# Performance work log

Measured on AMD Instinct MI355X. Metric: run time of the kernel, lower is better.

Reference implementation:

```python
import jax, jax.numpy as jnp
import numpy as np

B, N, T, F_FEAT, T_OUT = 256, 512, 12, 12, 12
HID = 3 * N           # 1536, LSTM hidden size
IN = N * F_FEAT       # 6144, LSTM input size


def setup_inputs() -> dict:
    key = jax.random.key(0)
    ks = jax.random.split(key, 8)
    stdv = 1.0 / np.sqrt(HID)
    u = lambda k, shape, s: jax.random.uniform(k, shape, jnp.float32, -s, s)
    return {
        "A_hat": jax.random.normal(ks[0], (N, N), jnp.float32),
        "X": jax.random.normal(ks[1], (B, N, T, F_FEAT), jnp.float32),
        "W_ih": u(ks[2], (4 * HID, IN), stdv),
        "W_hh": u(ks[3], (4 * HID, HID), stdv),
        "b_ih": u(ks[4], (4 * HID,), stdv),
        "b_hh": u(ks[5], (4 * HID,), stdv),
        "lin_W": u(ks[6], (T_OUT, 3 * T), 1.0 / np.sqrt(3 * T)),
        "lin_b": u(ks[7], (T_OUT,), 1.0 / np.sqrt(3 * T)),
    }


def reference(A_hat, X, W_ih, W_hh, b_ih, b_hh, lin_W, lin_b):
    # (B, N, T, F) -> (B, N*T, F) -> (F, B, N*T); loop axis is the feature dim
    out1 = X.reshape(B, N * T, F_FEAT).transpose(2, 0, 1)

    def step(carry, x_t):  # x_t: (B, N*T)
        h, c = carry
        gates = x_t @ W_ih.T + b_ih + h @ W_hh.T + b_hh  # (B, 4*HID)
        i, f, g, o = jnp.split(gates, 4, axis=-1)        # PyTorch gate order i,f,g,o
        c = jax.nn.sigmoid(f) * c + jax.nn.sigmoid(i) * jnp.tanh(g)
        h = jax.nn.sigmoid(o) * jnp.tanh(c)
        h = jnp.tanh(h)  # extra tanh applied in the original forward
        return (h, c), h

    init = (jnp.zeros((B, HID), X.dtype), jnp.zeros((B, HID), X.dtype))
    _, hs = jax.lax.scan(step, init, out1)          # (F, B, HID)
    al = hs.transpose(1, 2, 0)                      # (B, 3N, F) == torch.cat of unsqueezed states
    out2 = al.reshape(B, N, 3 * T)                  # (B, N, 3T)
    out3 = jax.nn.relu(out2) @ lin_W.T + lin_b      # (B, N, T_OUT)
    return out3
```

## Files before the change

kernel.cpp:

```cpp
#include <hip/hip_runtime.h>
#include <hip/hip_bf16.h>
#include <stdint.h>

typedef uint16_t u16;
typedef __attribute__((ext_vector_type(8))) __bf16 bf16x8;
typedef __attribute__((ext_vector_type(4))) float f32x4;
typedef __attribute__((ext_vector_type(4))) u16 u16x4;

#define BSZ   256
#define NN    512
#define TT    12
#define FF    12
#define HID   1536
#define INSZ  6144
#define GATES 6144
#define MROWS 3072

static __device__ __forceinline__ u16 f2bf(float x) {
  uint32_t u = __builtin_bit_cast(uint32_t, x);
  u += 0x7fffu + ((u >> 16) & 1u);
  return (u16)(u >> 16);
}

static __device__ __forceinline__ float sigm(float x) {
  return 1.0f / (1.0f + expf(-x));
}

__global__ void cvt_perm(const float* __restrict__ in, u16* __restrict__ out,
                         int ncol4) {
  long idx = (long)blockIdx.x * blockDim.x + threadIdx.x;
  int r  = (int)(idx / ncol4);
  int c4 = (int)(idx - (long)r * ncol4);
  int rp = ((r % HID) << 2) + r / HID;
  float4 v = ((const float4*)in)[idx];
  u16x4 w = { f2bf(v.x), f2bf(v.y), f2bf(v.z), f2bf(v.w) };
  ((u16x4*)out)[(size_t)rp * ncol4 + c4] = w;
}

__global__ void pack_x4(const float* __restrict__ X, u16* __restrict__ Ax) {
  int idx = blockIdx.x * blockDim.x + threadIdx.x;
  int b  = idx / (INSZ / 4);
  int k4 = idx - b * (INSZ / 4);
  const float* xp = X + (size_t)b * (INSZ * FF) + (size_t)k4 * (4 * FF);
  float4 v[12];
#pragma unroll
  for (int j = 0; j < 12; ++j) v[j] = ((const float4*)xp)[j];
  const float* vf = (const float*)v;
#pragma unroll
  for (int f = 0; f < FF; ++f) {
    u16x4 w = { f2bf(vf[0 * FF + f]), f2bf(vf[1 * FF + f]),
                f2bf(vf[2 * FF + f]), f2bf(vf[3 * FF + f]) };
    *(u16x4*)&Ax[(size_t)(f * BSZ + b) * INSZ + k4 * 4] = w;
  }
}

#define BM8 192
#define BN8 384
#define LDSA_SZ 24576
#define LDSB_SZ 49152
#define LDS_TOTAL (2 * (LDSA_SZ + LDSB_SZ))

#define GLL(src, dst)                                                          \
  __builtin_amdgcn_global_load_lds(                                            \
      (const __attribute__((address_space(1))) void*)(src),                    \
      (__attribute__((address_space(3))) void*)(dst), 16, 0, 0)

#define SBAR() asm volatile("s_barrier" ::: "memory")
#define SCHED_FENCE_DS() __builtin_amdgcn_sched_barrier(0x7F)
#define WAIT_LGKM0()                                                           \
  do {                                                                         \
    asm volatile("s_waitcnt lgkmcnt(0)" ::: "memory");                         \
    __builtin_amdgcn_sched_barrier(0);                                         \
  } while (0)

#define MFMA9(AF, BF, RO, CO)                                                  \
  do {                                                                         \
    __builtin_amdgcn_s_setprio(1);                                             \
    _Pragma("unroll") for (int i = 0; i < 3; ++i)                              \
        _Pragma("unroll") for (int j = 0; j < 3; ++j)                          \
            acc[RO + i][CO + j] = __builtin_amdgcn_mfma_f32_16x16x32_bf16(     \
                AF[i], BF[j], acc[RO + i][CO + j], 0, 0, 0);                   \
    __builtin_amdgcn_s_setprio(0);                                             \
  } while (0)

__global__ __launch_bounds__(512, 1) void gemm8p(
    const u16* __restrict__ A, const u16* __restrict__ Bt,
    const float* __restrict__ bi, const float* __restrict__ bh,
    float* __restrict__ C, int M, int N, int K) {
  extern __shared__ __align__(16) char lds[];
  const int tid  = threadIdx.x;
  const int lane = tid & 63;
  const int wid  = tid >> 6;
  const int wr   = wid >> 2;
  const int wc   = wid & 3;

  const int nbx  = N / BN8;
  const int cpx  = gridDim.x >> 3;
  const int orig = blockIdx.x;
  const int wgid = (orig & 7) * cpx + (orig >> 3);
  const int m0   = (wgid / nbx) * BM8;
  const int n0   = (wgid % nbx) * BN8;

  const int fr    = lane & 15;
  const int kb    = (lane >> 4) << 4;
  const int swz   = (fr & 7) << 4;
  const int colp0 = kb ^ swz;
  const int colp1 = (64 | kb) ^ swz;

  const int srow = tid >> 3;
  const int scb  = ((tid & 7) << 4) ^ ((srow & 7) << 4);
  const u16* gA = A  + (size_t)(m0 + srow) * K + (scb >> 1);
  const u16* gB = Bt + (size_t)(n0 + srow) * K + (scb >> 1);
  const int wdst = wid << 10;

  char* ldsA = lds;
  char* ldsB = lds + 2 * LDSA_SZ;
  char* aRowB = ldsA + (wr * 96 + fr) * 128;
  char* bRowB = ldsB + (wc * 96 + fr) * 128;

  f32x4 acc[6][6] = {};
  const int NT = K >> 6;

#pragma unroll
  for (int c = 0; c < 3; ++c) GLL(gA + (size_t)c * 64 * K, ldsA + c * 8192 + wdst);
#pragma unroll
  for (int c = 0; c < 6; ++c) GLL(gB + (size_t)c * 64 * K, ldsB + c * 8192 + wdst);

  for (int t = 0; t < NT; ++t) {
    const int p = t & 1;
    char* aRow = aRowB + p * LDSA_SZ;
    char* bRow = bRowB + p * LDSB_SZ;
    char* An = ldsA + (p ^ 1) * LDSA_SZ;
    char* Bn = ldsB + (p ^ 1) * LDSB_SZ;
    const u16* gAn = gA + (size_t)(t + 1) * 64;
    const u16* gBn = gB + (size_t)(t + 1) * 64;
    const bool pf = (t + 1 < NT);

    bf16x8 a0[2][3], a1[2][3], b0[2][3], b1[2][3];

    if (pf) {
#pragma unroll
      for (int c = 0; c < 3; ++c) GLL(gAn + (size_t)c * 64 * K, An + c * 8192 + wdst);
      asm volatile("s_waitcnt vmcnt(3)" ::: "memory");
    } else {
      asm volatile("s_waitcnt vmcnt(0)" ::: "memory");
    }
    SBAR();

#pragma unroll
    for (int i = 0; i < 3; ++i) {
      a0[0][i] = *(const bf16x8*)(aRow + i * 2048 + colp0);
      b0[0][i] = *(const bf16x8*)(bRow + i * 2048 + colp0);
    }
#pragma unroll
    for (int i = 0; i < 3; ++i) b1[0][i] = *(const bf16x8*)(bRow + (3 + i) * 2048 + colp0);
    MFMA9(a0[0], b0[0], 0, 0);
    if (pf) {
      GLL(gBn + (size_t)0 * 64 * K, Bn + 0 * 8192 + wdst);
      GLL(gBn + (size_t)1 * 64 * K, Bn + 1 * 8192 + wdst);
    }
    SCHED_FENCE_DS();

#pragma unroll
    for (int i = 0; i < 3; ++i) a1[0][i] = *(const bf16x8*)(aRow + (3 + i) * 2048 + colp0);
    MFMA9(a0[0], b1[0], 0, 3);
    if (pf) {
      GLL(gBn + (size_t)2 * 64 * K, Bn + 2 * 8192 + wdst);
      GLL(gBn + (size_t)3 * 64 * K, Bn + 3 * 8192 + wdst);
    }
    SCHED_FENCE_DS();

#pragma unroll
    for (int i = 0; i < 3; ++i) a0[1][i] = *(const bf16x8*)(aRow + i * 2048 + colp1);
    MFMA9(a1[0], b1[0], 3, 3);
    if (pf) {
      GLL(gBn + (size_t)4 * 64 * K, Bn + 4 * 8192 + wdst);
      GLL(gBn + (size_t)5 * 64 * K, Bn + 5 * 8192 + wdst);
    }
    SCHED_FENCE_DS();

#pragma unroll
    for (int i = 0; i < 3; ++i) b0[1][i] = *(const bf16x8*)(bRow + i * 2048 + colp1);
    MFMA9(a1[0], b0[0], 3, 0);
    SCHED_FENCE_DS();

#pragma unroll
    for (int i = 0; i < 3; ++i) b1[1][i] = *(const bf16x8*)(bRow + (3 + i) * 2048 + colp1);
    MFMA9(a0[1], b0[1], 0, 0);
    SCHED_FENCE_DS();

#pragma unroll
    for (int i = 0; i < 3; ++i) a1[1][i] = *(const bf16x8*)(aRow + (3 + i) * 2048 + colp1);
    MFMA9(a0[1], b1[1], 0, 3);
    SCHED_FENCE_DS();

    MFMA9(a1[1], b1[1], 3, 3);
    MFMA9(a1[1], b0[1], 3, 0);

    SBAR();
  }

  const int r0 = (lane >> 4) << 2;
  const int cc = lane & 15;
#pragma unroll
  for (int j = 0; j < 6; ++j) {
    const int col = n0 + wc * 96 + j * 16 + cc;
    const int oc  = (col & 3) * HID + (col >> 2);
    const float bv = bi[oc] + bh[oc];
#pragma unroll
    for (int i = 0; i < 6; ++i) {
      const size_t rbase = (size_t)(m0 + wr * 96 + i * 16 + r0) * N + col;
#pragma unroll
      for (int r = 0; r < 4; ++r)
        C[rbase + (size_t)r * N] = acc[i][j][r] + bv;
    }
  }
}

__global__ __launch_bounds__(256, 4) void gemm_cell(
    const u16* __restrict__ hbf_in,
    const u16* __restrict__ Whhb,
    const float* __restrict__ XW_f,
    float* __restrict__ cbuf,
    u16* __restrict__ hbf_out,
    float* __restrict__ hs_f) {
  __shared__ __align__(16) char lds[24576];
  const int tid  = threadIdx.x;
  const int lane = tid & 63;
  const int wid  = tid >> 6;
  const int wr   = wid >> 1;
  const int wc   = wid & 1;

  const int orig = blockIdx.x;
  const int xcd  = orig & 7;
  const int jj   = orig >> 3;
  const int n0   = (12 * xcd + (jj >> 3)) * 64;
  const int m0   = (jj & 7) * 32;
  const int K    = HID;

  const int fr    = lane & 15;
  const int kb    = (lane >> 4) << 4;
  const int swz   = (fr & 7) << 4;
  const int colp0 = kb ^ swz;
  const int colp1 = (64 | kb) ^ swz;

  const int srow = tid >> 3;
  const int scb  = ((tid & 7) << 4) ^ ((srow & 7) << 4);
  const u16* gA = hbf_in + (size_t)(m0 + srow) * K + (scb >> 1);
  const u16* gB = Whhb   + (size_t)(n0 + srow) * K + (scb >> 1);
  const int wdst = wid << 10;

  char* ldsA = lds;
  char* ldsB = lds + 8192;
  char* aRowB = ldsA + (wr * 16 + fr) * 128;
  char* bRowB = ldsB + (wc * 32 + fr) * 128;

  f32x4 acc[2] = {};
  const int NT = K >> 6;

  GLL(gA,                  ldsA + wdst);
  GLL(gB,                  ldsB + wdst);
  GLL(gB + (size_t)32 * K, ldsB + 4096 + wdst);

  for (int t = 0; t < NT; ++t) {
    const int p = t & 1;
    char* aRow = aRowB + p * 4096;
    char* bRow = bRowB + p * 8192;
    char* An = ldsA + (p ^ 1) * 4096;
    char* Bn = ldsB + (p ^ 1) * 8192;
    const u16* gAn = gA + (size_t)(t + 1) * 64;
    const u16* gBn = gB + (size_t)(t + 1) * 64;

    if (t + 1 < NT) {
      GLL(gAn,                  An + wdst);
      GLL(gBn,                  Bn + wdst);
      GLL(gBn + (size_t)32 * K, Bn + 4096 + wdst);
      asm volatile("s_waitcnt vmcnt(3)" ::: "memory");
    } else {
      asm volatile("s_waitcnt vmcnt(0)" ::: "memory");
    }
    SBAR();

    bf16x8 a[2], b[2][2];
    a[0] = *(const bf16x8*)(aRow + colp0);
    a[1] = *(const bf16x8*)(aRow + colp1);
#pragma unroll
    for (int j = 0; j < 2; ++j) {
      b[0][j] = *(const bf16x8*)(bRow + j * 2048 + colp0);
      b[1][j] = *(const bf16x8*)(bRow + j * 2048 + colp1);
    }
    WAIT_LGKM0();
    __builtin_amdgcn_s_setprio(1);
#pragma unroll
    for (int k = 0; k < 2; ++k)
#pragma unroll
      for (int j = 0; j < 2; ++j)
        acc[j] = __builtin_amdgcn_mfma_f32_16x16x32_bf16(a[k], b[k][j], acc[j], 0, 0, 0);
    __builtin_amdgcn_s_setprio(0);
    SBAR();
  }

  float* sacc = (float*)lds;
  const int r0 = (lane >> 4) << 2;
  const int cc = lane & 15;
#pragma unroll
  for (int j = 0; j < 2; ++j) {
    const int ml = wr * 16 + r0;
    const int nl = wc * 32 + j * 16 + cc;
#pragma unroll
    for (int r = 0; r < 4; ++r)
      sacc[(ml + r) * 68 + nl] = acc[j][r];
  }
  __syncthreads();

  for (int it = tid; it < 512; it += 256) {
    const int bl = it >> 4;
    const int jl = it & 15;
    const int b  = m0 + bl;
    const int jg = (n0 >> 2) + jl;
    const float4 hw = *(const float4*)&sacc[bl * 68 + jl * 4];
    const float4 xw = *(const float4*)&XW_f[(size_t)b * GATES + n0 + jl * 4];
    const float gi = xw.x + hw.x;
    const float gf = xw.y + hw.y;
    const float gg = xw.z + hw.z;
    const float go = xw.w + hw.w;
    const int cidx = b * HID + jg;
    const float cp = cbuf[cidx];
    const float cv = sigm(gf) * cp + sigm(gi) * tanhf(gg);
    const float h  = tanhf(sigm(go) * tanhf(cv));
    cbuf[cidx]    = cv;
    hbf_out[cidx] = f2bf(h);
    hs_f[cidx]    = h;
  }
}

__global__ void cell_first(const float* __restrict__ XW,
                           float* __restrict__ cbuf,
                           u16* __restrict__ hbf_out,
                           float* __restrict__ hs_f) {
  int it = blockIdx.x * blockDim.x + threadIdx.x;
  int b = it / HID;
  int j = it - b * HID;
  const float4 xw = *(const float4*)&XW[(size_t)b * GATES + 4 * j];
  const float cv = sigm(xw.x) * tanhf(xw.z);
  const float h  = tanhf(sigm(xw.w) * tanhf(cv));
  cbuf[it]    = cv;
  hbf_out[it] = f2bf(h);
  hs_f[it]    = h;
}

__global__ __launch_bounds__(256) void final_k(const float* __restrict__ hs,
                                               const float* __restrict__ lin_W,
                                               const float* __restrict__ lin_b,
                                               float* __restrict__ out) {
  __shared__ float Wsh[12 * 36];
  __shared__ float bsh[12];
  for (int i = threadIdx.x; i < 12 * 36; i += blockDim.x) Wsh[i] = lin_W[i];
  if (threadIdx.x < 12) bsh[threadIdx.x] = lin_b[threadIdx.x];
  __syncthreads();

  int idx = blockIdx.x * blockDim.x + threadIdx.x;
  int b = idx >> 9;
  int n = idx & 511;

  float acc[12];
#pragma unroll
  for (int o = 0; o < 12; ++o) acc[o] = bsh[o];

#pragma unroll
  for (int kk = 0; kk < 3; ++kk)
#pragma unroll
    for (int f = 0; f < 12; ++f) {
      float v = hs[(size_t)(f * BSZ + b) * HID + 3 * n + kk];
      v = fmaxf(v, 0.0f);
      int j = 12 * kk + f;
#pragma unroll
      for (int o = 0; o < 12; ++o) acc[o] += v * Wsh[o * 36 + j];
    }

#pragma unroll
  for (int o = 0; o < 12; ++o) out[(size_t)idx * 12 + o] = acc[o];
}

extern "C" void kernel_launch(void* const* d_in, const int* in_sizes, int n_in,
                              void* d_out, int out_size, void* d_ws, size_t ws_size,
                              hipStream_t stream) {
  (void)in_sizes; (void)n_in; (void)out_size; (void)ws_size;
  const float* X     = (const float*)d_in[1];
  const float* W_ih  = (const float*)d_in[2];
  const float* W_hh  = (const float*)d_in[3];
  const float* b_ih  = (const float*)d_in[4];
  const float* b_hh  = (const float*)d_in[5];
  const float* lin_W = (const float*)d_in[6];
  const float* lin_b = (const float*)d_in[7];
  float* out = (float*)d_out;

  char* p = (char*)d_ws;
  u16*   Ax   = (u16*)p;   p += (size_t)MROWS * INSZ * 2;
  u16*   Wihb = (u16*)p;   p += (size_t)GATES * INSZ * 2;
  u16*   Whhb = (u16*)p;   p += (size_t)GATES * HID * 2;
  float* XW   = (float*)p; p += (size_t)MROWS * GATES * 4;
  u16*   hbfA = (u16*)p;   p += (size_t)BSZ * HID * 2;
  u16*   hbfB = (u16*)p;   p += (size_t)BSZ * HID * 2;
  float* cbuf = (float*)p; p += (size_t)BSZ * HID * 4;
  float* hs   = (float*)p; p += (size_t)FF * BSZ * HID * 4;

  hipFuncSetAttribute((const void*)gemm8p,
                      hipFuncAttributeMaxDynamicSharedMemorySize, LDS_TOTAL);

  cvt_perm<<<(GATES * (INSZ / 4)) / 256, 256, 0, stream>>>(W_ih, Wihb, INSZ / 4);
  cvt_perm<<<(GATES * (HID / 4)) / 256, 256, 0, stream>>>(W_hh, Whhb, HID / 4);
  pack_x4<<<(BSZ * INSZ / 4) / 256, 256, 0, stream>>>(X, Ax);

  gemm8p<<<256, 512, LDS_TOTAL, stream>>>(Ax, Wihb, b_ih, b_hh, XW,
                                          MROWS, GATES, INSZ);

  u16* bufs[2] = { hbfA, hbfB };
  cell_first<<<(BSZ * HID) / 256, 256, 0, stream>>>(XW, cbuf, bufs[0], hs);
  for (int f = 1; f < FF; ++f) {
    gemm_cell<<<768, 256, 0, stream>>>(
        bufs[(f - 1) & 1], Whhb, XW + (size_t)f * BSZ * GATES, cbuf,
        bufs[f & 1], hs + (size_t)f * BSZ * HID);
  }

  final_k<<<(BSZ * NN) / 256, 256, 0, stream>>>(hs, lin_W, lin_b, out);
}
```

Before: 427.7 us.

## Software-pipeline big GEMM MFMA tail across iterations and store hidden states as bf16

The input-projection GEMM main loop is restructured so the last two MFMA groups of each K-step are deferred into the next iteration. This lets them overlap with the next tile's LDS reads and global prefetch instead of sitting at the end before the barrier. Separately, hidden states are kept only as a bf16 history array, used both as the recurrent GEMM input and by the final linear layer. This removes the fp32 hs writes and the ping-pong buffers, and halves the traffic into final_k. The cost is extra live registers for the carried fragments, an explicit lgkmcnt wait, and bf16 rounding of the values fed to the output layer.

```diff
diff --git a/kernel.cpp b/kernel.cpp
--- a/kernel.cpp
+++ b/kernel.cpp
@@ -20,6 +20,10 @@
   uint32_t u = __builtin_bit_cast(uint32_t, x);
   u += 0x7fffu + ((u >> 16) & 1u);
   return (u16)(u >> 16);
+}
+
+static __device__ __forceinline__ float bf2f(u16 x) {
+  return __builtin_bit_cast(float, (uint32_t)x << 16);
 }
 
 static __device__ __forceinline__ float sigm(float x) {
@@ -126,6 +130,8 @@
 #pragma unroll
   for (int c = 0; c < 6; ++c) GLL(gB + (size_t)c * 64 * K, ldsB + c * 8192 + wdst);
 
+  bf16x8 a1o[3], b1o[3], b0o[3];
+
   for (int t = 0; t < NT; ++t) {
     const int p = t & 1;
     char* aRow = aRowB + p * LDSA_SZ;
@@ -136,7 +142,8 @@
     const u16* gBn = gB + (size_t)(t + 1) * 64;
     const bool pf = (t + 1 < NT);
 
-    bf16x8 a0[2][3], a1[2][3], b0[2][3], b1[2][3];
+    bf16x8 a0k0[3], b0k0[3], b1k0[3], a1k0[3];
+    bf16x8 a0k1[3], b0k1[3], b1k1[3], a1k1[3];
 
     if (pf) {
 #pragma unroll
@@ -149,12 +156,15 @@
 
 #pragma unroll
     for (int i = 0; i < 3; ++i) {
-      a0[0][i] = *(const bf16x8*)(aRow + i * 2048 + colp0);
-      b0[0][i] = *(const bf16x8*)(bRow + i * 2048 + colp0);
-    }
-#pragma unroll
-    for (int i = 0; i < 3; ++i) b1[0][i] = *(const bf16x8*)(bRow + (3 + i) * 2048 + colp0);
-    MFMA9(a0[0], b0[0], 0, 0);
+      a0k0[i] = *(const bf16x8*)(aRow + i * 2048 + colp0);
+      b0k0[i] = *(const bf16x8*)(bRow + i * 2048 + colp0);
+    }
+    if (t > 0) MFMA9(a1o, b1o, 3, 3);
+    SCHED_FENCE_DS();
+
+#pragma unroll
+    for (int i = 0; i < 3; ++i) b1k0[i] = *(const bf16x8*)(bRow + (3 + i) * 2048 + colp0);
+    if (t > 0) MFMA9(a1o, b0o, 3, 0);
     if (pf) {
       GLL(gBn + (size_t)0 * 64 * K, Bn + 0 * 8192 + wdst);
       GLL(gBn + (size_t)1 * 64 * K, Bn + 1 * 8192 + wdst);
@@ -162,8 +172,8 @@
     SCHED_FENCE_DS();
 
 #pragma unroll
-    for (int i = 0; i < 3; ++i) a1[0][i] = *(const bf16x8*)(aRow + (3 + i) * 2048 + colp0);
-    MFMA9(a0[0], b1[0], 0, 3);
+    for (int i = 0; i < 3; ++i) a1k0[i] = *(const bf16x8*)(aRow + (3 + i) * 2048 + colp0);
+    MFMA9(a0k0, b0k0, 0, 0);
     if (pf) {
       GLL(gBn + (size_t)2 * 64 * K, Bn + 2 * 8192 + wdst);
       GLL(gBn + (size_t)3 * 64 * K, Bn + 3 * 8192 + wdst);
@@ -171,8 +181,8 @@
     SCHED_FENCE_DS();
 
 #pragma unroll
-    for (int i = 0; i < 3; ++i) a0[1][i] = *(const bf16x8*)(aRow + i * 2048 + colp1);
-    MFMA9(a1[0], b1[0], 3, 3);
+    for (int i = 0; i < 3; ++i) a0k1[i] = *(const bf16x8*)(aRow + i * 2048 + colp1);
+    MFMA9(a0k0, b1k0, 0, 3);
     if (pf) {
       GLL(gBn + (size_t)4 * 64 * K, Bn + 4 * 8192 + wdst);
       GLL(gBn + (size_t)5 * 64 * K, Bn + 5 * 8192 + wdst);
@@ -180,25 +190,30 @@
     SCHED_FENCE_DS();
 
 #pragma unroll
-    for (int i = 0; i < 3; ++i) b0[1][i] = *(const bf16x8*)(bRow + i * 2048 + colp1);
-    MFMA9(a1[0], b0[0], 3, 0);
-    SCHED_FENCE_DS();
-
-#pragma unroll
-    for (int i = 0; i < 3; ++i) b1[1][i] = *(const bf16x8*)(bRow + (3 + i) * 2048 + colp1);
-    MFMA9(a0[1], b0[1], 0, 0);
-    SCHED_FENCE_DS();
-
-#pragma unroll
-    for (int i = 0; i < 3; ++i) a1[1][i] = *(const bf16x8*)(aRow + (3 + i) * 2048 + colp1);
-    MFMA9(a0[1], b1[1], 0, 3);
-    SCHED_FENCE_DS();
-
-    MFMA9(a1[1], b1[1], 3, 3);
-    MFMA9(a1[1], b0[1], 3, 0);
-
+    for (int i = 0; i < 3; ++i) b0k1[i] = *(const bf16x8*)(bRow + i * 2048 + colp1);
+    MFMA9(a1k0, b1k0, 3, 3);
+    SCHED_FENCE_DS();
+
+#pragma unroll
+    for (int i = 0; i < 3; ++i) b1k1[i] = *(const bf16x8*)(bRow + (3 + i) * 2048 + colp1);
+    MFMA9(a1k0, b0k0, 3, 0);
+    SCHED_FENCE_DS();
+
+#pragma unroll
+    for (int i = 0; i < 3; ++i) a1k1[i] = *(const bf16x8*)(aRow + (3 + i) * 2048 + colp1);
+    MFMA9(a0k1, b0k1, 0, 0);
+    SCHED_FENCE_DS();
+
+    MFMA9(a0k1, b1k1, 0, 3);
+#pragma unroll
+    for (int i = 0; i < 3; ++i) { a1o[i] = a1k1[i]; b1o[i] = b1k1[i]; b0o[i] = b0k1[i]; }
+
+    asm volatile("s_waitcnt lgkmcnt(0)" ::: "memory");
     SBAR();
   }
+
+  MFMA9(a1o, b1o, 3, 3);
+  MFMA9(a1o, b0o, 3, 0);
 
   const int r0 = (lane >> 4) << 2;
   const int cc = lane & 15;
@@ -218,12 +233,11 @@
 }
 
 __global__ __launch_bounds__(256, 4) void gemm_cell(
-    const u16* __restrict__ hbf_in,
+    const u16* __restrict__ hs_in,
     const u16* __restrict__ Whhb,
     const float* __restrict__ XW_f,
     float* __restrict__ cbuf,
-    u16* __restrict__ hbf_out,
-    float* __restrict__ hs_f) {
+    u16* __restrict__ hs_out) {
   __shared__ __align__(16) char lds[24576];
   const int tid  = threadIdx.x;
   const int lane = tid & 63;
@@ -246,8 +260,8 @@
 
   const int srow = tid >> 3;
   const int scb  = ((tid & 7) << 4) ^ ((srow & 7) << 4);
-  const u16* gA = hbf_in + (size_t)(m0 + srow) * K + (scb >> 1);
-  const u16* gB = Whhb   + (size_t)(n0 + srow) * K + (scb >> 1);
+  const u16* gA = hs_in + (size_t)(m0 + srow) * K + (scb >> 1);
+  const u16* gB = Whhb  + (size_t)(n0 + srow) * K + (scb >> 1);
   const int wdst = wid << 10;
 
   char* ldsA = lds;
@@ -328,28 +342,25 @@
     const float cp = cbuf[cidx];
     const float cv = sigm(gf) * cp + sigm(gi) * tanhf(gg);
     const float h  = tanhf(sigm(go) * tanhf(cv));
-    cbuf[cidx]    = cv;
-    hbf_out[cidx] = f2bf(h);
-    hs_f[cidx]    = h;
+    cbuf[cidx]   = cv;
+    hs_out[cidx] = f2bf(h);
   }
 }
 
 __global__ void cell_first(const float* __restrict__ XW,
                            float* __restrict__ cbuf,
-                           u16* __restrict__ hbf_out,
-                           float* __restrict__ hs_f) {
+                           u16* __restrict__ hs_out) {
   int it = blockIdx.x * blockDim.x + threadIdx.x;
   int b = it / HID;
   int j = it - b * HID;
   const float4 xw = *(const float4*)&XW[(size_t)b * GATES + 4 * j];
   const float cv = sigm(xw.x) * tanhf(xw.z);
   const float h  = tanhf(sigm(xw.w) * tanhf(cv));
-  cbuf[it]    = cv;
-  hbf_out[it] = f2bf(h);
-  hs_f[it]    = h;
-}
-
-__global__ __launch_bounds__(256) void final_k(const float* __restrict__ hs,
+  cbuf[it]   = cv;
+  hs_out[it] = f2bf(h);
+}
+
+__global__ __launch_bounds__(256) void final_k(const u16* __restrict__ hs,
                                                const float* __restrict__ lin_W,
                                                const float* __restrict__ lin_b,
                                                float* __restrict__ out) {
@@ -371,7 +382,7 @@
   for (int kk = 0; kk < 3; ++kk)
 #pragma unroll
     for (int f = 0; f < 12; ++f) {
-      float v = hs[(size_t)(f * BSZ + b) * HID + 3 * n + kk];
+      float v = bf2f(hs[(size_t)(f * BSZ + b) * HID + 3 * n + kk]);
       v = fmaxf(v, 0.0f);
       int j = 12 * kk + f;
 #pragma unroll
@@ -400,10 +411,8 @@
   u16*   Wihb = (u16*)p;   p += (size_t)GATES * INSZ * 2;
   u16*   Whhb = (u16*)p;   p += (size_t)GATES * HID * 2;
   float* XW   = (float*)p; p += (size_t)MROWS * GATES * 4;
-  u16*   hbfA = (u16*)p;   p += (size_t)BSZ * HID * 2;
-  u16*   hbfB = (u16*)p;   p += (size_t)BSZ * HID * 2;
   float* cbuf = (float*)p; p += (size_t)BSZ * HID * 4;
-  float* hs   = (float*)p; p += (size_t)FF * BSZ * HID * 4;
+  u16*   hs   = (u16*)p;   p += (size_t)FF * BSZ * HID * 2;
 
   hipFuncSetAttribute((const void*)gemm8p,
                       hipFuncAttributeMaxDynamicSharedMemorySize, LDS_TOTAL);
@@ -415,12 +424,11 @@
   gemm8p<<<256, 512, LDS_TOTAL, stream>>>(Ax, Wihb, b_ih, b_hh, XW,
                                           MROWS, GATES, INSZ);
 
-  u16* bufs[2] = { hbfA, hbfB };
-  cell_first<<<(BSZ * HID) / 256, 256, 0, stream>>>(XW, cbuf, bufs[0], hs);
+  const size_t S = (size_t)BSZ * HID;
+  cell_first<<<(BSZ * HID) / 256, 256, 0, stream>>>(XW, cbuf, hs);
   for (int f = 1; f < FF; ++f) {
     gemm_cell<<<768, 256, 0, stream>>>(
-        bufs[(f - 1) & 1], Whhb, XW + (size_t)f * BSZ * GATES, cbuf,
-        bufs[f & 1], hs + (size_t)f * BSZ * HID);
+        hs + (f - 1) * S, Whhb, XW + (size_t)f * BSZ * GATES, cbuf, hs + f * S);
   }
 
   final_k<<<(BSZ * NN) / 256, 256, 0, stream>>>(hs, lin_W, lin_b, out);
```

After: 419.5 us. Within noise of the previous version (-1.9%).
